# Optimization experiments

Measured on AMD Instinct MI355X. Metric: run time of the kernel, lower is better.

The kernel has to match this reference:

```python
import jax, jax.numpy as jnp
import numpy as np

N_NODES = 100000
NEG_SLOPE = 0.01  # F.leaky_relu default


def setup_inputs() -> dict:
    key = jax.random.key(0)
    k1, k2, k3, k4, k5 = jax.random.split(key, 5)
    x = jax.random.normal(k1, (N_NODES, 128), dtype=jnp.float32)
    edge_index = jax.random.randint(k2, (2, 1600000), 0, N_NODES, dtype=jnp.int64)
    # GCNConv linear weights (PyG: x @ W.T), bias added after aggregation
    W1 = jax.random.normal(k3, (128, 128), dtype=jnp.float32) * (1.0 / np.sqrt(128))
    b1 = jnp.zeros((128,), dtype=jnp.float32)
    W2 = jax.random.normal(k4, (128, 128), dtype=jnp.float32) * (1.0 / np.sqrt(128))
    b2 = jnp.zeros((128,), dtype=jnp.float32)
    return {"x": x, "edge_index": edge_index, "W1": W1, "b1": b1, "W2": W2, "b2": b2}


def _gcn_layer(x, W, b, src, dst, norm, self_w):
    # linear transform first (GCNConv order): h = x @ W.T
    h = x @ W.T
    # message passing: sum_j norm_ij * h_j  (edges) + self-loop term h_i / deg_i
    msg = h[src] * norm[:, None]                       # [E, F] gather (memory-bound)
    agg = jax.ops.segment_sum(msg, dst, num_segments=x.shape[0])
    out = agg + h * self_w[:, None] + b
    return out


def reference(x, edge_index, W1, b1, W2, b2):
    src = edge_index[0]
    dst = edge_index[1]
    n = x.shape[0]
    # gcn_norm with self-loops: deg_i = in-degree(dst) + 1
    deg = jax.ops.segment_sum(jnp.ones_like(dst, dtype=x.dtype), dst, num_segments=n) + 1.0
    deg_inv_sqrt = jax.lax.rsqrt(deg)
    norm = deg_inv_sqrt[src] * deg_inv_sqrt[dst]       # edge weights
    self_w = deg_inv_sqrt * deg_inv_sqrt               # self-loop weight = 1/deg

    h = _gcn_layer(x, W1, b1, src, dst, norm, self_w)
    h = jax.nn.leaky_relu(h, NEG_SLOPE)
    # dropout inactive (eval semantics)
    h = _gcn_layer(h, W2, b2, src, dst, norm, self_w)
    h = jax.nn.leaky_relu(h, NEG_SLOPE)
    return h
```

## Files before the change

### kernel.cpp

```cpp
#include <hip/hip_runtime.h>

#define F 128
#define NEG_SLOPE 0.01f
#define NPB 512
#define PMAX 256
#define HB 8192
#define BB 8192
#define CAP 12288

typedef _Float16 half8_t __attribute__((ext_vector_type(8)));
typedef float f32x4 __attribute__((ext_vector_type(4)));


__global__ __launch_bounds__(512) void zero_bcnt(int* __restrict__ bcnt,
                                                 int* __restrict__ bcur) {
    int tid = threadIdx.x;
    if (tid < PMAX) bcnt[tid] = 0;
    else bcur[tid - PMAX] = 0;
}

__global__ __launch_bounds__(256) void hist_kernel(const int* __restrict__ dst,
                                                   int* __restrict__ bcnt,
                                                   int E, int nP,
                                                   const float* __restrict__ W1,
                                                   const float* __restrict__ W2,
                                                   _Float16* __restrict__ W1h,
                                                   _Float16* __restrict__ W2h) {
    __shared__ int h[PMAX];
    int tid = threadIdx.x;
    int hb = gridDim.x - 32;
    if (blockIdx.x >= hb) {
        int i = (blockIdx.x - hb) * 256 + tid;
        const int n4 = F * F / 4;
        const float* in = (i < n4) ? W1 : W2;
        _Float16* out = (i < n4) ? W1h : W2h;
        int j = (i < n4) ? i : i - n4;
        float4 v = ((const float4*)in)[j];
        half8_t hx;
        hx[0] = (_Float16)v.x; hx[1] = (_Float16)v.y;
        hx[2] = (_Float16)v.z; hx[3] = (_Float16)v.w;
        *(int2*)&((_Float16*)out)[j * 4] = *(int2*)&hx;
        return;
    }
    if (tid < PMAX) h[tid] = 0;
    __syncthreads();
    int base = blockIdx.x * HB;
    for (int i = tid; i < HB && base + i < E; i += 256)
        atomicAdd(&h[dst[base + i] >> 9], 1);
    __syncthreads();
    if (tid < nP && h[tid]) atomicAdd(&bcnt[tid], h[tid]);
}

__global__ __launch_bounds__(256) void bin_kernel(const int* __restrict__ src,
                                                  const int* __restrict__ dst,
                                                  const int* __restrict__ bcnt,
                                                  int* __restrict__ bcur,
                                                  int* __restrict__ bbase,
                                                  int* __restrict__ binned,
                                                  int E, int nP) {
    __shared__ int hist[PMAX];
    __shared__ int lbase[PMAX];
    __shared__ int gbase[PMAX];
    __shared__ int cur[PMAX];
    __shared__ int sa[PMAX];
    __shared__ int sb[PMAX];
    __shared__ int buf[BB];
    __shared__ unsigned char b8[BB];
    int tid = threadIdx.x;
    int base = blockIdx.x * BB;
    int myE = E - base; if (myE > BB) myE = BB;

    hist[tid] = 0;
    __syncthreads();
    for (int i = tid; i < myE; i += 256)
        atomicAdd(&hist[dst[base + i] >> 9], 1);
    __syncthreads();
    {
        int v = (tid < nP) ? hist[tid] : 0;
        int run = v;
        sa[tid] = v;
        __syncthreads();
        for (int off = 1; off < PMAX; off <<= 1) {
            int add = (tid >= off) ? sa[tid - off] : 0;
            __syncthreads();
            run += add;
            sa[tid] = run;
            __syncthreads();
        }
        if (tid < nP) { lbase[tid] = run - v; cur[tid] = run - v; }
    }
    {
        int v = (tid < nP) ? bcnt[tid] : 0;
        int run = v;
        sb[tid] = v;
        __syncthreads();
        for (int off = 1; off < PMAX; off <<= 1) {
            int add = (tid >= off) ? sb[tid - off] : 0;
            __syncthreads();
            run += add;
            sb[tid] = run;
            __syncthreads();
        }
        int gexc = run - v;
        if (tid < nP) {
            if (blockIdx.x == 0) bbase[tid] = gexc;
            gbase[tid] = hist[tid] ? gexc + atomicAdd(&bcur[tid], hist[tid]) : 0;
        }
    }
    __syncthreads();
    for (int i = tid; i < myE; i += 256) {
        int d = dst[base + i], s = src[base + i];
        int b = d >> 9;
        int lp = atomicAdd(&cur[b], 1);
        buf[lp] = ((d & (NPB - 1)) << 17) | s;
        b8[lp] = (unsigned char)b;
    }
    __syncthreads();
    for (int j = tid; j < myE; j += 256) {
        int b = b8[j];
        binned[gbase[b] + (j - lbase[b])] = buf[j];
    }
}

__global__ __launch_bounds__(256) void csr_kernel(const int* __restrict__ binned,
                                                  const int* __restrict__ bcnt,
                                                  const int* __restrict__ bbase,
                                                  int* __restrict__ srcs,
                                                  int* __restrict__ offs,
                                                  float* __restrict__ dis, int N) {
    __shared__ int cnt[NPB];
    __shared__ int tmp[NPB];
    __shared__ int cur[NPB];
    __shared__ int buf[CAP];
    int tid = threadIdx.x;
    int b = blockIdx.x;
    int ebase = bbase[b];
    int count = bcnt[b];
    int lo = b << 9;
    cnt[tid] = 0;
    cnt[tid + 256] = 0;
    __syncthreads();
    for (int j = tid; j < count; j += 256)
        atomicAdd(&cnt[binned[ebase + j] >> 17], 1);
    __syncthreads();
    int j0 = tid, j1 = tid + 256;
    int v0 = cnt[j0], v1 = cnt[j1];
    tmp[j0] = v0; tmp[j1] = v1;
    __syncthreads();
    for (int off = 1; off < NPB; off <<= 1) {
        int t0 = tmp[j0] + (j0 >= off ? tmp[j0 - off] : 0);
        int t1 = tmp[j1] + (j1 >= off ? tmp[j1 - off] : 0);
        __syncthreads();
        tmp[j0] = t0; tmp[j1] = t1;
        __syncthreads();
    }
    int e0 = tmp[j0] - v0, e1 = tmp[j1] - v1;
    cur[j0] = e0; cur[j1] = e1;
    int n0 = lo + j0, n1 = lo + j1;
    if (n0 < N) { offs[n0] = ebase + e0; dis[n0] = rsqrtf((float)v0 + 1.0f); }
    if (n1 < N) { offs[n1] = ebase + e1; dis[n1] = rsqrtf((float)v1 + 1.0f); }
    __syncthreads();
    for (int j = tid; j < count; j += 256) {
        int rec = binned[ebase + j];
        int pos = atomicAdd(&cur[rec >> 17], 1);
        int s = rec & 0x1FFFF;
        if (pos < CAP) buf[pos] = s; else srcs[ebase + pos] = s;
    }
    __syncthreads();
    int lim = count < CAP ? count : CAP;
    for (int j = tid; j < lim; j += 256)
        srcs[ebase + j] = buf[j];
}


__global__ __launch_bounds__(256) void gemm_a32(const float* __restrict__ A,
                                                const _Float16* __restrict__ Wh,
                                                const float* __restrict__ dis,
                                                _Float16* __restrict__ out,
                                                int ntiles) {
    int wave = threadIdx.x >> 6;
    int lane = threadIdx.x & 63;
    int tile = blockIdx.x * 4 + wave;
    if (tile >= ntiles) return;
    int m = lane & 15, quad = lane >> 4;
    const float* arow = A + (size_t)tile * 16 * F;
    half8_t afrag[4];
#pragma unroll
    for (int c = 0; c < 4; ++c) {
        float4 t0 = *(const float4*)&arow[m * F + c * 32 + quad * 8];
        float4 t1 = *(const float4*)&arow[m * F + c * 32 + quad * 8 + 4];
        afrag[c][0] = (_Float16)t0.x; afrag[c][1] = (_Float16)t0.y;
        afrag[c][2] = (_Float16)t0.z; afrag[c][3] = (_Float16)t0.w;
        afrag[c][4] = (_Float16)t1.x; afrag[c][5] = (_Float16)t1.y;
        afrag[c][6] = (_Float16)t1.z; afrag[c][7] = (_Float16)t1.w;
    }
    f32x4 acc[8];
#pragma unroll
    for (int t = 0; t < 8; ++t) acc[t] = (f32x4){0.f, 0.f, 0.f, 0.f};
#pragma unroll
    for (int c = 0; c < 4; ++c) {
#pragma unroll
        for (int t = 0; t < 8; ++t) {
            half8_t bfrag = *(const half8_t*)&Wh[(t * 16 + m) * F + c * 32 + quad * 8];
            acc[t] = __builtin_amdgcn_mfma_f32_16x16x32_f16(afrag[c], bfrag, acc[t],
                                                            0, 0, 0);
        }
    }
    float d[4];
#pragma unroll
    for (int r = 0; r < 4; ++r) d[r] = dis[tile * 16 + quad * 4 + r];
    _Float16* orow = out + (size_t)tile * 16 * F;
#pragma unroll
    for (int t = 0; t < 8; ++t)
#pragma unroll
        for (int r = 0; r < 4; ++r)
            orow[(quad * 4 + r) * F + t * 16 + m] = (_Float16)(acc[t][r] * d[r]);
}


__global__ __launch_bounds__(128) void agg_gemm16(const half8_t* __restrict__ h8,
                                                  const float* __restrict__ dis,
                                                  const float* __restrict__ bias,
                                                  const _Float16* __restrict__ Wh,
                                                  const int* __restrict__ srcs,
                                                  const int* __restrict__ offs,
                                                  _Float16* __restrict__ out,
                                                  int n, int E) {
    __shared__ _Float16 Af[16 * F];
    int tile = blockIdx.x;
    int w = threadIdx.x >> 6;
    int lane = threadIdx.x & 63;
    int g = lane >> 4;
    int fo = lane & 15;
    float4 b0 = ((const float4*)bias)[fo * 2];
    float4 b1v = ((const float4*)bias)[fo * 2 + 1];

    for (int i = 0; i < 8; ++i) {
        int row = w * 8 + i;
        int node = tile * 16 + row;
        float acc[8];
#pragma unroll
        for (int j = 0; j < 8; ++j) acc[j] = 0.f;
        int beg = 0, end = 0;
        float di = 0.f;
        half8_t hv = {};
        if (node < n) {
            beg = offs[node];
            end = (node + 1 < n) ? offs[node + 1] : E;
            di = dis[node];
            hv = h8[(size_t)node * 16 + fo];
        }
        if (beg < end) {
            int i0 = beg + g, i1 = beg + 4 + g;
            int s0 = srcs[i0 < end ? i0 : beg];
            int s1 = srcs[i1 < end ? i1 : beg];
            float w0 = (i0 < end) ? 1.f : 0.f;
            float w1 = (i1 < end) ? 1.f : 0.f;
            for (int e = beg; e < end; e += 8) {
                int ns0 = s0, ns1 = s1;
                float nw0 = 0.f, nw1 = 0.f;
                if (e + 8 < end) {
                    int j0 = e + 8 + g, j1 = e + 12 + g;
                    ns0 = srcs[j0 < end ? j0 : beg];
                    ns1 = srcs[j1 < end ? j1 : beg];
                    nw0 = (j0 < end) ? 1.f : 0.f;
                    nw1 = (j1 < end) ? 1.f : 0.f;
                }
                half8_t a0 = h8[(size_t)s0 * 16 + fo];
                half8_t a1 = h8[(size_t)s1 * 16 + fo];
#pragma unroll
                for (int j = 0; j < 8; ++j)
                    acc[j] += w0 * (float)a0[j] + w1 * (float)a1[j];
                s0 = ns0; s1 = ns1; w0 = nw0; w1 = nw1;
            }
        }
#pragma unroll
        for (int j = 0; j < 8; ++j) {
            acc[j] += __shfl_xor(acc[j], 16);
            acc[j] += __shfl_xor(acc[j], 32);
        }
        if (lane < 16) {
            half8_t o = {};
            if (node < n) {
                acc[0] = di * (acc[0] + (float)hv[0]) + b0.x;
                acc[1] = di * (acc[1] + (float)hv[1]) + b0.y;
                acc[2] = di * (acc[2] + (float)hv[2]) + b0.z;
                acc[3] = di * (acc[3] + (float)hv[3]) + b0.w;
                acc[4] = di * (acc[4] + (float)hv[4]) + b1v.x;
                acc[5] = di * (acc[5] + (float)hv[5]) + b1v.y;
                acc[6] = di * (acc[6] + (float)hv[6]) + b1v.z;
                acc[7] = di * (acc[7] + (float)hv[7]) + b1v.w;
#pragma unroll
                for (int j = 0; j < 8; ++j) {
                    float v = (acc[j] > 0.f) ? acc[j] : acc[j] * NEG_SLOPE;
                    o[j] = (_Float16)v;
                }
            }
            int cs = fo ^ (row & 7);
            *(half8_t*)&Af[row * F + cs * 8] = o;
        }
    }
    __syncthreads();

    int m = fo, quad = g;
    half8_t afrag[4];
#pragma unroll
    for (int c = 0; c < 4; ++c) {
        int j = c * 4 + quad;
        afrag[c] = *(const half8_t*)&Af[m * F + (j ^ (m & 7)) * 8];
    }
    float d[4];
#pragma unroll
    for (int r = 0; r < 4; ++r) {
        int node = tile * 16 + quad * 4 + r;
        d[r] = (node < n) ? dis[node] : 0.f;
    }
#pragma unroll
    for (int s = 0; s < 4; ++s) {
        int t = w * 4 + s;
        f32x4 acc2 = (f32x4){0.f, 0.f, 0.f, 0.f};
#pragma unroll
        for (int c = 0; c < 4; ++c) {
            half8_t bfrag = *(const half8_t*)&Wh[(t * 16 + m) * F + c * 32 + quad * 8];
            acc2 = __builtin_amdgcn_mfma_f32_16x16x32_f16(afrag[c], bfrag, acc2,
                                                          0, 0, 0);
        }
#pragma unroll
        for (int r = 0; r < 4; ++r) {
            int node = tile * 16 + quad * 4 + r;
            if (node < n)
                out[(size_t)node * F + t * 16 + m] = (_Float16)(acc2[r] * d[r]);
        }
    }
}


#define AGG_BODY(H8)                                                           \
    int node = blockIdx.x * 4 + (threadIdx.x >> 6);                            \
    int lane = threadIdx.x & 63;                                               \
    if (node >= n) return;                                                     \
    int g = lane >> 4;                                                         \
    int fo = lane & 15;                                                        \
    int beg = offs[node];                                                      \
    int end = (node + 1 < n) ? offs[node + 1] : E;                             \
    float di = dis[node];                                                      \
    half8_t hv = H8[(size_t)node * 16 + fo];                                   \
    float4 b0 = ((const float4*)bias)[fo * 2];                                 \
    float4 b1v = ((const float4*)bias)[fo * 2 + 1];                            \
    float acc[8];                                                              \
    _Pragma("unroll") for (int j = 0; j < 8; ++j) acc[j] = 0.f;                \
    if (beg < end) {                                                           \
        int i0 = beg + g, i1 = beg + 4 + g;                                    \
        int s0 = srcs[i0 < end ? i0 : beg];                                    \
        int s1 = srcs[i1 < end ? i1 : beg];                                    \
        float w0 = (i0 < end) ? 1.f : 0.f;                                     \
        float w1 = (i1 < end) ? 1.f : 0.f;                                     \
        for (int e = beg; e < end; e += 8) {                                   \
            int ns0 = s0, ns1 = s1;                                            \
            float nw0 = 0.f, nw1 = 0.f;                                        \
            if (e + 8 < end) {                                                 \
                int j0 = e + 8 + g, j1 = e + 12 + g;                           \
                ns0 = srcs[j0 < end ? j0 : beg];                               \
                ns1 = srcs[j1 < end ? j1 : beg];                               \
                nw0 = (j0 < end) ? 1.f : 0.f;                                  \
                nw1 = (j1 < end) ? 1.f : 0.f;                                  \
            }                                                                  \
            half8_t a0 = H8[(size_t)s0 * 16 + fo];                             \
            half8_t a1 = H8[(size_t)s1 * 16 + fo];                             \
            _Pragma("unroll") for (int j = 0; j < 8; ++j)                      \
                acc[j] += w0 * (float)a0[j] + w1 * (float)a1[j];               \
            s0 = ns0; s1 = ns1; w0 = nw0; w1 = nw1;                            \
        }                                                                      \
    }                                                                          \
    _Pragma("unroll") for (int j = 0; j < 8; ++j) {                            \
        acc[j] += __shfl_xor(acc[j], 16);                                      \
        acc[j] += __shfl_xor(acc[j], 32);                                      \
    }                                                                          \
    if (lane >= 16) return;                                                    \
    acc[0] = di * (acc[0] + (float)hv[0]) + b0.x;                              \
    acc[1] = di * (acc[1] + (float)hv[1]) + b0.y;                              \
    acc[2] = di * (acc[2] + (float)hv[2]) + b0.z;                              \
    acc[3] = di * (acc[3] + (float)hv[3]) + b0.w;                              \
    acc[4] = di * (acc[4] + (float)hv[4]) + b1v.x;                             \
    acc[5] = di * (acc[5] + (float)hv[5]) + b1v.y;                             \
    acc[6] = di * (acc[6] + (float)hv[6]) + b1v.z;                             \
    acc[7] = di * (acc[7] + (float)hv[7]) + b1v.w;                             \
    _Pragma("unroll") for (int j = 0; j < 8; ++j)                              \
        acc[j] = (acc[j] > 0.f) ? acc[j] : acc[j] * NEG_SLOPE;

__global__ __launch_bounds__(256) void agg_to_f(const half8_t* __restrict__ h8,
                                                const float* __restrict__ dis,
                                                const float* __restrict__ bias,
                                                const int* __restrict__ srcs,
                                                const int* __restrict__ offs,
                                                float* __restrict__ out,
                                                int n, int E) {
    AGG_BODY(h8)
    float4 o0 = make_float4(acc[0], acc[1], acc[2], acc[3]);
    float4 o1 = make_float4(acc[4], acc[5], acc[6], acc[7]);
    ((float4*)out)[(size_t)node * 32 + fo * 2] = o0;
    ((float4*)out)[(size_t)node * 32 + fo * 2 + 1] = o1;
}


static inline size_t alup(size_t x) { return (x + 255) & ~(size_t)255; }

extern "C" void kernel_launch(void* const* d_in, const int* in_sizes, int n_in,
                              void* d_out, int out_size, void* d_ws, size_t ws_size,
                              hipStream_t stream) {
    const float* x  = (const float*)d_in[0];
    const int*   ei = (const int*)d_in[1];
    const float* W1 = (const float*)d_in[2];
    const float* b1 = (const float*)d_in[3];
    const float* W2 = (const float*)d_in[4];
    const float* b2 = (const float*)d_in[5];
    float* out = (float*)d_out;

    const int N = in_sizes[0] / F;
    const int E = in_sizes[1] / 2;
    const int* src = ei;
    const int* dst = ei + E;

    char* p = (char*)d_ws;
    int*      bcnt   = (int*)p;      p += alup(PMAX * 4);
    int*      bbase  = (int*)p;      p += alup(PMAX * 4);
    int*      bcur   = (int*)p;      p += alup(PMAX * 4);
    float*    dis    = (float*)p;    p += alup((size_t)N * 4);
    int*      offs   = (int*)p;      p += alup((size_t)N * 4);
    int*      binned = (int*)p;      p += alup((size_t)E * 4);
    int*      srcs   = (int*)p;      p += alup((size_t)E * 4);
    _Float16* g      = (_Float16*)p; p += alup((size_t)N * F * 2);
    _Float16* hh     = (_Float16*)p; p += alup((size_t)N * F * 2);
    _Float16* W1h    = (_Float16*)p; p += alup((size_t)F * F * 2);
    _Float16* W2h    = (_Float16*)p; p += alup((size_t)F * F * 2);

    const int nP = (N + NPB - 1) / NPB;
    const int ntiles = (N + 15) / 16;
    const int gemm_grid = (ntiles + 3) / 4;
    const int agg_grid = (N + 3) / 4;

    zero_bcnt<<<1, 512, 0, stream>>>(bcnt, bcur);
    hist_kernel<<<(E + HB - 1) / HB + 32, 256, 0, stream>>>(dst, bcnt, E, nP,
                                                            W1, W2, W1h, W2h);
    bin_kernel<<<(E + BB - 1) / BB, 256, 0, stream>>>(src, dst, bcnt, bcur,
                                                      bbase, binned, E, nP);
    csr_kernel<<<nP, 256, 0, stream>>>(binned, bcnt, bbase, srcs, offs, dis, N);

    gemm_a32<<<gemm_grid, 256, 0, stream>>>(x, W1h, dis, hh, ntiles);
    agg_gemm16<<<ntiles, 128, 0, stream>>>((const half8_t*)hh, dis, b1, W2h,
                                           srcs, offs, g, N, E);
    agg_to_f<<<agg_grid, 256, 0, stream>>>((const half8_t*)g, dis, b2, srcs,
                                           offs, out, N, E);
}
```

Before: 324.6 us.

## Widen agg_gemm16 to four waves, transpose MFMA for vector stores, add nontemporal hints

```diff
diff --git a/kernel.cpp b/kernel.cpp
--- a/kernel.cpp
+++ b/kernel.cpp
@@ -9,6 +9,7 @@
 #define CAP 12288
 
 typedef _Float16 half8_t __attribute__((ext_vector_type(8)));
+typedef _Float16 half4_t __attribute__((ext_vector_type(4)));
 typedef float f32x4 __attribute__((ext_vector_type(4)));
 
 
@@ -187,12 +188,14 @@
     half8_t afrag[4];
 #pragma unroll
     for (int c = 0; c < 4; ++c) {
-        float4 t0 = *(const float4*)&arow[m * F + c * 32 + quad * 8];
-        float4 t1 = *(const float4*)&arow[m * F + c * 32 + quad * 8 + 4];
-        afrag[c][0] = (_Float16)t0.x; afrag[c][1] = (_Float16)t0.y;
-        afrag[c][2] = (_Float16)t0.z; afrag[c][3] = (_Float16)t0.w;
-        afrag[c][4] = (_Float16)t1.x; afrag[c][5] = (_Float16)t1.y;
-        afrag[c][6] = (_Float16)t1.z; afrag[c][7] = (_Float16)t1.w;
+        f32x4 t0 = __builtin_nontemporal_load(
+            (const f32x4*)&arow[m * F + c * 32 + quad * 8]);
+        f32x4 t1 = __builtin_nontemporal_load(
+            (const f32x4*)&arow[m * F + c * 32 + quad * 8 + 4]);
+        afrag[c][0] = (_Float16)t0[0]; afrag[c][1] = (_Float16)t0[1];
+        afrag[c][2] = (_Float16)t0[2]; afrag[c][3] = (_Float16)t0[3];
+        afrag[c][4] = (_Float16)t1[0]; afrag[c][5] = (_Float16)t1[1];
+        afrag[c][6] = (_Float16)t1[2]; afrag[c][7] = (_Float16)t1[3];
     }
     f32x4 acc[8];
 #pragma unroll
@@ -218,7 +221,7 @@
 }
 
 
-__global__ __launch_bounds__(128) void agg_gemm16(const half8_t* __restrict__ h8,
+__global__ __launch_bounds__(256) void agg_gemm16(const half8_t* __restrict__ h8,
                                                   const float* __restrict__ dis,
                                                   const float* __restrict__ bias,
                                                   const _Float16* __restrict__ Wh,
@@ -235,8 +238,9 @@
     float4 b0 = ((const float4*)bias)[fo * 2];
     float4 b1v = ((const float4*)bias)[fo * 2 + 1];
 
-    for (int i = 0; i < 8; ++i) {
-        int row = w * 8 + i;
+#pragma unroll
+    for (int i = 0; i < 4; ++i) {
+        int row = w * 4 + i;
         int node = tile * 16 + row;
         float acc[8];
 #pragma unroll
@@ -303,90 +307,30 @@
     __syncthreads();
 
     int m = fo, quad = g;
-    half8_t afrag[4];
-#pragma unroll
-    for (int c = 0; c < 4; ++c) {
-        int j = c * 4 + quad;
-        afrag[c] = *(const half8_t*)&Af[m * F + (j ^ (m & 7)) * 8];
-    }
-    float d[4];
-#pragma unroll
-    for (int r = 0; r < 4; ++r) {
-        int node = tile * 16 + quad * 4 + r;
-        d[r] = (node < n) ? dis[node] : 0.f;
-    }
-#pragma unroll
-    for (int s = 0; s < 4; ++s) {
-        int t = w * 4 + s;
+    half8_t bfragA[4];
+#pragma unroll
+    for (int c = 0; c < 4; ++c)
+        bfragA[c] = *(const half8_t*)&Af[fo * F + ((c * 4 + quad) ^ (fo & 7)) * 8];
+    int onode = tile * 16 + fo;
+    float di2 = (onode < n) ? dis[onode] : 0.f;
+#pragma unroll
+    for (int s = 0; s < 2; ++s) {
+        int t = w * 2 + s;
         f32x4 acc2 = (f32x4){0.f, 0.f, 0.f, 0.f};
 #pragma unroll
         for (int c = 0; c < 4; ++c) {
-            half8_t bfrag = *(const half8_t*)&Wh[(t * 16 + m) * F + c * 32 + quad * 8];
-            acc2 = __builtin_amdgcn_mfma_f32_16x16x32_f16(afrag[c], bfrag, acc2,
+            half8_t afragW = *(const half8_t*)&Wh[(t * 16 + m) * F + c * 32 + quad * 8];
+            acc2 = __builtin_amdgcn_mfma_f32_16x16x32_f16(afragW, bfragA[c], acc2,
                                                           0, 0, 0);
         }
-#pragma unroll
-        for (int r = 0; r < 4; ++r) {
-            int node = tile * 16 + quad * 4 + r;
-            if (node < n)
-                out[(size_t)node * F + t * 16 + m] = (_Float16)(acc2[r] * d[r]);
-        }
-    }
-}
-
-
-#define AGG_BODY(H8)                                                           \
-    int node = blockIdx.x * 4 + (threadIdx.x >> 6);                            \
-    int lane = threadIdx.x & 63;                                               \
-    if (node >= n) return;                                                     \
-    int g = lane >> 4;                                                         \
-    int fo = lane & 15;                                                        \
-    int beg = offs[node];                                                      \
-    int end = (node + 1 < n) ? offs[node + 1] : E;                             \
-    float di = dis[node];                                                      \
-    half8_t hv = H8[(size_t)node * 16 + fo];                                   \
-    float4 b0 = ((const float4*)bias)[fo * 2];                                 \
-    float4 b1v = ((const float4*)bias)[fo * 2 + 1];                            \
-    float acc[8];                                                              \
-    _Pragma("unroll") for (int j = 0; j < 8; ++j) acc[j] = 0.f;                \
-    if (beg < end) {                                                           \
-        int i0 = beg + g, i1 = beg + 4 + g;                                    \
-        int s0 = srcs[i0 < end ? i0 : beg];                                    \
-        int s1 = srcs[i1 < end ? i1 : beg];                                    \
-        float w0 = (i0 < end) ? 1.f : 0.f;                                     \
-        float w1 = (i1 < end) ? 1.f : 0.f;                                     \
-        for (int e = beg; e < end; e += 8) {                                   \
-            int ns0 = s0, ns1 = s1;                                            \
-            float nw0 = 0.f, nw1 = 0.f;                                        \
-            if (e + 8 < end) {                                                 \
-                int j0 = e + 8 + g, j1 = e + 12 + g;                           \
-                ns0 = srcs[j0 < end ? j0 : beg];                               \
-                ns1 = srcs[j1 < end ? j1 : beg];                               \
-                nw0 = (j0 < end) ? 1.f : 0.f;                                  \
-                nw1 = (j1 < end) ? 1.f : 0.f;                                  \
-            }                                                                  \
-            half8_t a0 = H8[(size_t)s0 * 16 + fo];                             \
-            half8_t a1 = H8[(size_t)s1 * 16 + fo];                             \
-            _Pragma("unroll") for (int j = 0; j < 8; ++j)                      \
-                acc[j] += w0 * (float)a0[j] + w1 * (float)a1[j];               \
-            s0 = ns0; s1 = ns1; w0 = nw0; w1 = nw1;                            \
-        }                                                                      \
-    }                                                                          \
-    _Pragma("unroll") for (int j = 0; j < 8; ++j) {                            \
-        acc[j] += __shfl_xor(acc[j], 16);                                      \
-        acc[j] += __shfl_xor(acc[j], 32);                                      \
-    }                                                                          \
-    if (lane >= 16) return;                                                    \
-    acc[0] = di * (acc[0] + (float)hv[0]) + b0.x;                              \
-    acc[1] = di * (acc[1] + (float)hv[1]) + b0.y;                              \
-    acc[2] = di * (acc[2] + (float)hv[2]) + b0.z;                              \
-    acc[3] = di * (acc[3] + (float)hv[3]) + b0.w;                              \
-    acc[4] = di * (acc[4] + (float)hv[4]) + b1v.x;                             \
-    acc[5] = di * (acc[5] + (float)hv[5]) + b1v.y;                             \
-    acc[6] = di * (acc[6] + (float)hv[6]) + b1v.z;                             \
-    acc[7] = di * (acc[7] + (float)hv[7]) + b1v.w;                             \
-    _Pragma("unroll") for (int j = 0; j < 8; ++j)                              \
-        acc[j] = (acc[j] > 0.f) ? acc[j] : acc[j] * NEG_SLOPE;
+        half4_t o4;
+#pragma unroll
+        for (int r = 0; r < 4; ++r) o4[r] = (_Float16)(acc2[r] * di2);
+        if (onode < n)
+            *(half4_t*)&out[(size_t)onode * F + t * 16 + quad * 4] = o4;
+    }
+}
+
 
 __global__ __launch_bounds__(256) void agg_to_f(const half8_t* __restrict__ h8,
                                                 const float* __restrict__ dis,
@@ -395,11 +339,65 @@
                                                 const int* __restrict__ offs,
                                                 float* __restrict__ out,
                                                 int n, int E) {
-    AGG_BODY(h8)
-    float4 o0 = make_float4(acc[0], acc[1], acc[2], acc[3]);
-    float4 o1 = make_float4(acc[4], acc[5], acc[6], acc[7]);
-    ((float4*)out)[(size_t)node * 32 + fo * 2] = o0;
-    ((float4*)out)[(size_t)node * 32 + fo * 2 + 1] = o1;
+    int node = blockIdx.x * 4 + (threadIdx.x >> 6);
+    int lane = threadIdx.x & 63;
+    if (node >= n) return;
+    int g = lane >> 4;
+    int fo = lane & 15;
+    int beg = offs[node];
+    int end = (node + 1 < n) ? offs[node + 1] : E;
+    float di = dis[node];
+    half8_t hv = h8[(size_t)node * 16 + fo];
+    float4 b0 = ((const float4*)bias)[fo * 2];
+    float4 b1v = ((const float4*)bias)[fo * 2 + 1];
+    float acc[8];
+#pragma unroll
+    for (int j = 0; j < 8; ++j) acc[j] = 0.f;
+    if (beg < end) {
+        int i0 = beg + g, i1 = beg + 4 + g;
+        int s0 = __builtin_nontemporal_load(&srcs[i0 < end ? i0 : beg]);
+        int s1 = __builtin_nontemporal_load(&srcs[i1 < end ? i1 : beg]);
+        float w0 = (i0 < end) ? 1.f : 0.f;
+        float w1 = (i1 < end) ? 1.f : 0.f;
+        for (int e = beg; e < end; e += 8) {
+            int ns0 = s0, ns1 = s1;
+            float nw0 = 0.f, nw1 = 0.f;
+            if (e + 8 < end) {
+                int j0 = e + 8 + g, j1 = e + 12 + g;
+                ns0 = __builtin_nontemporal_load(&srcs[j0 < end ? j0 : beg]);
+                ns1 = __builtin_nontemporal_load(&srcs[j1 < end ? j1 : beg]);
+                nw0 = (j0 < end) ? 1.f : 0.f;
+                nw1 = (j1 < end) ? 1.f : 0.f;
+            }
+            half8_t a0 = h8[(size_t)s0 * 16 + fo];
+            half8_t a1 = h8[(size_t)s1 * 16 + fo];
+#pragma unroll
+            for (int j = 0; j < 8; ++j)
+                acc[j] += w0 * (float)a0[j] + w1 * (float)a1[j];
+            s0 = ns0; s1 = ns1; w0 = nw0; w1 = nw1;
+        }
+    }
+#pragma unroll
+    for (int j = 0; j < 8; ++j) {
+        acc[j] += __shfl_xor(acc[j], 16);
+        acc[j] += __shfl_xor(acc[j], 32);
+    }
+    if (lane >= 16) return;
+    acc[0] = di * (acc[0] + (float)hv[0]) + b0.x;
+    acc[1] = di * (acc[1] + (float)hv[1]) + b0.y;
+    acc[2] = di * (acc[2] + (float)hv[2]) + b0.z;
+    acc[3] = di * (acc[3] + (float)hv[3]) + b0.w;
+    acc[4] = di * (acc[4] + (float)hv[4]) + b1v.x;
+    acc[5] = di * (acc[5] + (float)hv[5]) + b1v.y;
+    acc[6] = di * (acc[6] + (float)hv[6]) + b1v.z;
+    acc[7] = di * (acc[7] + (float)hv[7]) + b1v.w;
+#pragma unroll
+    for (int j = 0; j < 8; ++j)
+        acc[j] = (acc[j] > 0.f) ? acc[j] : acc[j] * NEG_SLOPE;
+    f32x4 o0 = (f32x4){acc[0], acc[1], acc[2], acc[3]};
+    f32x4 o1 = (f32x4){acc[4], acc[5], acc[6], acc[7]};
+    __builtin_nontemporal_store(o0, (f32x4*)out + (size_t)node * 32 + fo * 2);
+    __builtin_nontemporal_store(o1, (f32x4*)out + (size_t)node * 32 + fo * 2 + 1);
 }
 
 
@@ -447,7 +445,7 @@
     csr_kernel<<<nP, 256, 0, stream>>>(binned, bcnt, bbase, srcs, offs, dis, N);
 
     gemm_a32<<<gemm_grid, 256, 0, stream>>>(x, W1h, dis, hh, ntiles);
-    agg_gemm16<<<ntiles, 128, 0, stream>>>((const half8_t*)hh, dis, b1, W2h,
+    agg_gemm16<<<ntiles, 256, 0, stream>>>((const half8_t*)hh, dis, b1, W2h,
                                            srcs, offs, g, N, E);
     agg_to_f<<<agg_grid, 256, 0, stream>>>((const half8_t*)g, dis, b2, srcs,
                                            offs, out, N, E);
```

Measured after the change: 329.7 us. About the same (+1.6%).
